# Kernel tuning notes

Measured on AMD Instinct MI355X. Metric: run time of the kernel, lower is better.

The kernel has to match this reference:

```python
import jax, jax.numpy as jnp
import numpy as np

B, T, H, L = 256, 1024, 64, 5  # batch, seq_len, hidden_size, num_layers


def setup_inputs() -> dict:
    key = jax.random.key(0)
    ks = jax.random.split(key, 10)
    s = 1.0 / np.sqrt(H)  # PyTorch LSTM/Linear uniform init bound

    def u(k, shape):
        return jax.random.uniform(k, shape, jnp.float32, -s, s)

    return {
        "x": jax.random.normal(ks[0], (B, T, 1), jnp.float32),
        "w_ih0": u(ks[1], (4 * H, 1)),          # layer 0 input weights (input_size=1)
        "w_ih_rest": u(ks[2], (L - 1, 4 * H, H)),  # layers 1..4 input weights
        "w_hh": u(ks[3], (L, 4 * H, H)),
        "b_ih": u(ks[4], (L, 4 * H)),
        "b_hh": u(ks[5], (L, 4 * H)),
        "W1": u(ks[6], (H, H)),
        "b1": u(ks[7], (H,)),
        "W2": u(ks[8], (1, H)),
        "b2": u(ks[9], (1,)),
        "future": 0,
    }


def _lstm_layer(x, w_ih, w_hh, b_ih, b_hh):
    # x: [B, T, in]; PyTorch gate order i, f, g, o
    gx = jnp.einsum('bti,gi->btg', x, w_ih) + b_ih  # precompute input projections [B,T,4H]
    h0 = jnp.zeros((x.shape[0], w_hh.shape[1]), x.dtype)

    def step(carry, gxt):
        h, c = carry
        gates = gxt + h @ w_hh.T + b_hh  # [B,4H]
        i, f, g, o = jnp.split(gates, 4, axis=-1)
        c = jax.nn.sigmoid(f) * c + jax.nn.sigmoid(i) * jnp.tanh(g)
        h = jax.nn.sigmoid(o) * jnp.tanh(c)
        return (h, c), h

    _, hs = jax.lax.scan(step, (h0, h0), jnp.swapaxes(gx, 0, 1))  # scan over time
    return jnp.swapaxes(hs, 0, 1)  # [B,T,H]


def _model(x, w_ih0, w_ih_rest, w_hh, b_ih, b_hh, W1, b1, W2, b2):
    # 5-layer LSTM (inter-layer dropout=0.1 is inactive in eval mode)
    h = _lstm_layer(x, w_ih0, w_hh[0], b_ih[0], b_hh[0])
    for l in range(1, w_hh.shape[0]):
        h = _lstm_layer(h, w_ih_rest[l - 1], w_hh[l], b_ih[l], b_hh[l])
    h = jax.nn.relu(h)
    h = jax.nn.relu(h @ W1.T + b1)
    return h @ W2.T + b2  # [B,T,1]


def reference(x, w_ih0, w_ih_rest, w_hh, b_ih, b_hh, W1, b1, W2, b2, future):
    out = None
    for _ in range(future + 1):
        out = _model(x, w_ih0, w_ih_rest, w_hh, b_ih, b_hh, W1, b1, W2, b2)
        x = jnp.concatenate([x, out[:, -1:, :]], axis=1)
    return out
```

## Files before the change

kernel.cpp:

```cpp
#include <hip/hip_runtime.h>

#define B_ 256
#define T_ 1024
#define H_ 64

typedef float f32x2 __attribute__((ext_vector_type(2)));
typedef float f32x4 __attribute__((ext_vector_type(4)));

__device__ __forceinline__ float fast_sigmoid(float x) {
    float e = __builtin_amdgcn_exp2f(-1.4426950408889634f * x);
    return __builtin_amdgcn_rcpf(1.0f + e);
}
__device__ __forceinline__ float fast_tanh(float x) {
    float e = __builtin_amdgcn_exp2f(2.8853900817779268f * x);
    return 1.0f - 2.0f * __builtin_amdgcn_rcpf(1.0f + e);
}

template<int CTRL>
__device__ __forceinline__ float dpp_addf(float v) {
    int vi = __builtin_bit_cast(int, v);
    int sh = __builtin_amdgcn_update_dpp(0, vi, CTRL, 0xF, 0xF, true);
    return v + __builtin_bit_cast(float, sh);
}

__device__ __forceinline__ void block_sync_lds() {
    asm volatile("s_waitcnt lgkmcnt(0)\n\ts_barrier" ::: "memory");
}

__device__ __forceinline__ float hsum4(f32x4 v) { return (v.x + v.y) + (v.z + v.w); }

__device__ __forceinline__ void load_w_heavy(const float* __restrict__ w_ih,
                                             const float* __restrict__ w_hh,
                                             int j, int kc, f32x4 wt[4][8]) {
    #pragma unroll
    for (int r = 0; r < 4; ++r) {
        const int row = r * H_ + j;
        const float* base = (kc < 2) ? (w_ih + row * H_ + kc * 32)
                                     : (w_hh + row * H_ + (kc - 2) * 32);
        #pragma unroll
        for (int q = 0; q < 8; ++q)
            wt[r][q] = *(const f32x4*)(base + 4 * q);
    }
    #pragma unroll
    for (int r = 0; r < 4; ++r)
        #pragma unroll
        for (int q = 0; q < 8; ++q)
            asm volatile("" : "+v"(wt[r][q]));
}

__device__ __forceinline__ void dot4x32(const float* chunk, const f32x4 wt[4][8],
                                        float acc[4]) {
    const f32x4* xv = (const f32x4*)chunk;
    f32x4 a0 = {0,0,0,0}, a1 = {0,0,0,0}, a2 = {0,0,0,0}, a3 = {0,0,0,0};
    #pragma unroll
    for (int q = 0; q < 8; ++q) {
        f32x4 hq = xv[q];
        a0 = __builtin_elementwise_fma(wt[0][q], hq, a0);
        a1 = __builtin_elementwise_fma(wt[1][q], hq, a1);
        a2 = __builtin_elementwise_fma(wt[2][q], hq, a2);
        a3 = __builtin_elementwise_fma(wt[3][q], hq, a3);
    }
    acc[0] = hsum4(a0); acc[1] = hsum4(a1);
    acc[2] = hsum4(a2); acc[3] = hsum4(a3);
}

__global__ __attribute__((amdgpu_flat_work_group_size(768, 768)))
void lstm_tri012(const float* __restrict__ x,
                 float* __restrict__ hout,
                 const float* __restrict__ w_ih0,
                 const float* __restrict__ whh0,
                 const float* __restrict__ bih0, const float* __restrict__ bhh0,
                 const float* __restrict__ wih1, const float* __restrict__ whh1,
                 const float* __restrict__ bih1, const float* __restrict__ bhh1,
                 const float* __restrict__ wih2, const float* __restrict__ whh2,
                 const float* __restrict__ bih2, const float* __restrict__ bhh2)
{
    const int b    = blockIdx.x;
    const int tid  = threadIdx.x;
    const int role = tid >> 8;
    const int loc  = tid & 255;
    const int kc   = loc & 3;
    const int j    = loc >> 2;

    __shared__ __align__(16) float bufL0[2][80];
    __shared__ __align__(16) float bufL1[2][144];
    __shared__ __align__(16) float bufL2[2][144];

    f32x4 wt[4][8];
    float bias0 = 0.f, bias1 = 0.f, bias2 = 0.f, bias3 = 0.f;
    float w00 = 0.f, w01 = 0.f, w02 = 0.f, w03 = 0.f;

    if (role == 0) {
        #pragma unroll
        for (int r = 0; r < 4; ++r) {
            const int row = r * H_ + j;
            const float* base = whh0 + row * H_ + kc * 16;
            #pragma unroll
            for (int q = 0; q < 4; ++q)
                wt[r][q] = *(const f32x4*)(base + 4 * q);
        }
        #pragma unroll
        for (int r = 0; r < 4; ++r)
            #pragma unroll
            for (int q = 0; q < 4; ++q)
                asm volatile("" : "+v"(wt[r][q]));
        if (kc == 0) {
            bias0 = bih0[0*H_+j] + bhh0[0*H_+j];
            bias1 = bih0[1*H_+j] + bhh0[1*H_+j];
            bias2 = bih0[2*H_+j] + bhh0[2*H_+j];
            bias3 = bih0[3*H_+j] + bhh0[3*H_+j];
            w00 = w_ih0[0*H_+j]; w01 = w_ih0[1*H_+j];
            w02 = w_ih0[2*H_+j]; w03 = w_ih0[3*H_+j];
        }
    } else {
        const float* wih = (role == 1) ? wih1 : wih2;
        const float* whh = (role == 1) ? whh1 : whh2;
        const float* bih = (role == 1) ? bih1 : bih2;
        const float* bhh = (role == 1) ? bhh1 : bhh2;
        load_w_heavy(wih, whh, j, kc, wt);
        if (kc == 0) {
            bias0 = bih[0*H_+j] + bhh[0*H_+j];
            bias1 = bih[1*H_+j] + bhh[1*H_+j];
            bias2 = bih[2*H_+j] + bhh[2*H_+j];
            bias3 = bih[3*H_+j] + bhh[3*H_+j];
        }
    }
    float c_st = 0.f;
    float xt = (role == 0) ? x[(long)b * T_] : 0.f;

    float (*myBuf)[144] = (role == 1) ? bufL1 : bufL2;

    if (loc < H_) {
        const int u = loc;
        if (role == 0)      bufL0[0][(u >> 4) * 20 + (u & 15)] = 0.f;
        else if (role == 1) bufL1[1][(2 + (u >> 5)) * 36 + (u & 31)] = 0.f;
        else                bufL2[0][(2 + (u >> 5)) * 36 + (u & 31)] = 0.f;
    }
    block_sync_lds();

    for (int s = 0; s <= T_ + 1; ++s) {
        const int rb = s & 1, wb = rb ^ 1;
        const bool active = (role == 0) ? (s < T_)
                          : (role == 1) ? (s >= 1 && s <= T_)
                                        : (s >= 2);
        if (active) {
            if (role == 0) {
                float xn = 0.f;
                if (s + 1 < T_) xn = x[(long)b * T_ + s + 1];
                const f32x4* xv = (const f32x4*)&bufL0[rb][kc * 20];
                f32x4 h0 = xv[0], h1 = xv[1], h2 = xv[2], h3 = xv[3];
                f32x4 a0 = {0,0,0,0}, a1 = {0,0,0,0}, a2 = {0,0,0,0}, a3 = {0,0,0,0};
                a0 = __builtin_elementwise_fma(wt[0][0], h0, a0);
                a1 = __builtin_elementwise_fma(wt[1][0], h0, a1);
                a2 = __builtin_elementwise_fma(wt[2][0], h0, a2);
                a3 = __builtin_elementwise_fma(wt[3][0], h0, a3);
                a0 = __builtin_elementwise_fma(wt[0][1], h1, a0);
                a1 = __builtin_elementwise_fma(wt[1][1], h1, a1);
                a2 = __builtin_elementwise_fma(wt[2][1], h1, a2);
                a3 = __builtin_elementwise_fma(wt[3][1], h1, a3);
                a0 = __builtin_elementwise_fma(wt[0][2], h2, a0);
                a1 = __builtin_elementwise_fma(wt[1][2], h2, a1);
                a2 = __builtin_elementwise_fma(wt[2][2], h2, a2);
                a3 = __builtin_elementwise_fma(wt[3][2], h2, a3);
                a0 = __builtin_elementwise_fma(wt[0][3], h3, a0);
                a1 = __builtin_elementwise_fma(wt[1][3], h3, a1);
                a2 = __builtin_elementwise_fma(wt[2][3], h3, a2);
                a3 = __builtin_elementwise_fma(wt[3][3], h3, a3);
                float acc0 = hsum4(a0), acc1 = hsum4(a1);
                float acc2 = hsum4(a2), acc3 = hsum4(a3);
                acc0 = dpp_addf<0xB1>(acc0); acc1 = dpp_addf<0xB1>(acc1);
                acc2 = dpp_addf<0xB1>(acc2); acc3 = dpp_addf<0xB1>(acc3);
                acc0 = dpp_addf<0x4E>(acc0); acc1 = dpp_addf<0x4E>(acc1);
                acc2 = dpp_addf<0x4E>(acc2); acc3 = dpp_addf<0x4E>(acc3);
                if (kc == 0) {
                    float i_ = fast_sigmoid(acc0 + bias0 + w00 * xt);
                    float f_ = fast_sigmoid(acc1 + bias1 + w01 * xt);
                    float g_ = fast_tanh   (acc2 + bias2 + w02 * xt);
                    float o_ = fast_sigmoid(acc3 + bias3 + w03 * xt);
                    c_st = f_ * c_st + i_ * g_;
                    float h = o_ * fast_tanh(c_st);
                    bufL0[wb][(j >> 4) * 20 + (j & 15)] = h;
                    bufL1[wb][(j >> 5) * 36 + (j & 31)] = h;
                }
                xt = xn;
            } else {
                float acc[4];
                dot4x32(&myBuf[rb][kc * 36], wt, acc);
                acc[0] = dpp_addf<0xB1>(acc[0]); acc[1] = dpp_addf<0xB1>(acc[1]);
                acc[2] = dpp_addf<0xB1>(acc[2]); acc[3] = dpp_addf<0xB1>(acc[3]);
                acc[0] = dpp_addf<0x4E>(acc[0]); acc[1] = dpp_addf<0x4E>(acc[1]);
                acc[2] = dpp_addf<0x4E>(acc[2]); acc[3] = dpp_addf<0x4E>(acc[3]);
                if (kc == 0) {
                    float i_ = fast_sigmoid(acc[0] + bias0);
                    float f_ = fast_sigmoid(acc[1] + bias1);
                    float g_ = fast_tanh   (acc[2] + bias2);
                    float o_ = fast_sigmoid(acc[3] + bias3);
                    c_st = f_ * c_st + i_ * g_;
                    float h = o_ * fast_tanh(c_st);
                    myBuf[wb][(2 + (j >> 5)) * 36 + (j & 31)] = h;
                    if (role == 1)
                        bufL2[wb][(j >> 5) * 36 + (j & 31)] = h;
                    else
                        hout[((long)b * T_ + (s - 2)) * H_ + j] = h;
                }
            }
        }
        block_sync_lds();
    }
}

__global__ __attribute__((amdgpu_flat_work_group_size(512, 512)))
void lstm_pair34(const float* __restrict__ xin,
                 float* __restrict__ hout,
                 const float* __restrict__ wih3, const float* __restrict__ whh3,
                 const float* __restrict__ bih3, const float* __restrict__ bhh3,
                 const float* __restrict__ wih4, const float* __restrict__ whh4,
                 const float* __restrict__ bih4, const float* __restrict__ bhh4)
{
    const int b    = blockIdx.x;
    const int tid  = threadIdx.x;
    const int role = tid >> 8;
    const int loc  = tid & 255;
    const int kc   = loc & 3;
    const int j    = loc >> 2;

    __shared__ __align__(16) float bufL3[2][144];
    __shared__ __align__(16) float bufL4[2][144];

    const float* wih = (role == 0) ? wih3 : wih4;
    const float* whh = (role == 0) ? whh3 : whh4;
    const float* bih = (role == 0) ? bih3 : bih4;
    const float* bhh = (role == 0) ? bhh3 : bhh4;
    float (*myBuf)[144] = (role == 0) ? bufL3 : bufL4;

    f32x4 wt[4][8];
    load_w_heavy(wih, whh, j, kc, wt);

    float bias0 = 0.f, bias1 = 0.f, bias2 = 0.f, bias3 = 0.f;
    if (kc == 0) {
        bias0 = bih[0*H_+j] + bhh[0*H_+j];
        bias1 = bih[1*H_+j] + bhh[1*H_+j];
        bias2 = bih[2*H_+j] + bhh[2*H_+j];
        bias3 = bih[3*H_+j] + bhh[3*H_+j];
    }
    float c_st = 0.f;

    if (tid < H_) {
        const int u = tid;
        bufL3[0][(u >> 5) * 36 + (u & 31)] = xin[(long)b * T_ * H_ + u];
        bufL3[0][(2 + (u >> 5)) * 36 + (u & 31)] = 0.f;
    } else if (tid < 128) {
        const int u = tid - 64;
        bufL4[1][(2 + (u >> 5)) * 36 + (u & 31)] = 0.f;
    }
    block_sync_lds();

    for (int s = 0; s <= T_; ++s) {
        const int rb = s & 1, wb = rb ^ 1;
        const bool active = (role == 0) ? (s < T_) : (s >= 1);
        if (active) {
            float xn = 0.f;
            if (role == 0 && kc == 1 && s + 1 < T_)
                xn = xin[((long)b * T_ + s + 1) * H_ + j];

            float acc[4];
            dot4x32(&myBuf[rb][kc * 36], wt, acc);
            acc[0] = dpp_addf<0xB1>(acc[0]); acc[1] = dpp_addf<0xB1>(acc[1]);
            acc[2] = dpp_addf<0xB1>(acc[2]); acc[3] = dpp_addf<0xB1>(acc[3]);
            acc[0] = dpp_addf<0x4E>(acc[0]); acc[1] = dpp_addf<0x4E>(acc[1]);
            acc[2] = dpp_addf<0x4E>(acc[2]); acc[3] = dpp_addf<0x4E>(acc[3]);

            if (kc == 0) {
                float i_ = fast_sigmoid(acc[0] + bias0);
                float f_ = fast_sigmoid(acc[1] + bias1);
                float g_ = fast_tanh   (acc[2] + bias2);
                float o_ = fast_sigmoid(acc[3] + bias3);
                c_st = f_ * c_st + i_ * g_;
                float h = o_ * fast_tanh(c_st);
                myBuf[wb][(2 + (j >> 5)) * 36 + (j & 31)] = h;
                if (role == 0)
                    bufL4[wb][(j >> 5) * 36 + (j & 31)] = h;
                else
                    hout[((long)b * T_ + (s - 1)) * H_ + j] = h;
            }
            if (role == 0 && kc == 1)
                bufL3[wb][(j >> 5) * 36 + (j & 31)] = xn;
        }
        block_sync_lds();
    }
}

__global__ __launch_bounds__(256)
void mlp_head_v2(const float* __restrict__ hbuf,
                 const float* __restrict__ W1,
                 const float* __restrict__ b1,
                 const float* __restrict__ W2,
                 const float* __restrict__ b2,
                 float* __restrict__ out)
{
    const long r = (long)blockIdx.x * 256 + threadIdx.x;

    float row[H_];
    const float4* src = (const float4*)(hbuf + r * H_);
    #pragma unroll
    for (int q = 0; q < 16; ++q) {
        float4 v = src[q];
        row[4*q+0] = fmaxf(v.x, 0.f); row[4*q+1] = fmaxf(v.y, 0.f);
        row[4*q+2] = fmaxf(v.z, 0.f); row[4*q+3] = fmaxf(v.w, 0.f);
    }
    #pragma unroll
    for (int q = 0; q < 16; ++q)
        asm volatile("" : "+v"(row[4*q]), "+v"(row[4*q+1]),
                         "+v"(row[4*q+2]), "+v"(row[4*q+3]));

    float acc = b2[0];
    for (int jj = 0; jj < H_; ++jj) {
        const float* wrow = W1 + jj * H_;
        float s0 = 0.f, s1 = 0.f, s2 = 0.f, s3 = 0.f;
        #pragma unroll
        for (int q = 0; q < 16; ++q) {
            s0 += row[4*q+0] * wrow[4*q+0];
            s1 += row[4*q+1] * wrow[4*q+1];
            s2 += row[4*q+2] * wrow[4*q+2];
            s3 += row[4*q+3] * wrow[4*q+3];
        }
        float y = fmaxf(b1[jj] + (s0 + s1) + (s2 + s3), 0.f);
        acc += y * W2[jj];
    }
    out[r] = acc;
}

extern "C" void kernel_launch(void* const* d_in, const int* in_sizes, int n_in,
                              void* d_out, int out_size, void* d_ws, size_t ws_size,
                              hipStream_t stream) {
    const float* x     = (const float*)d_in[0];
    const float* w_ih0 = (const float*)d_in[1];
    const float* w_ihr = (const float*)d_in[2];
    const float* w_hh  = (const float*)d_in[3];
    const float* b_ih  = (const float*)d_in[4];
    const float* b_hh  = (const float*)d_in[5];
    const float* W1    = (const float*)d_in[6];
    const float* b1    = (const float*)d_in[7];
    const float* W2    = (const float*)d_in[8];
    const float* b2    = (const float*)d_in[9];

    float* out = (float*)d_out;
    float* buf = (float*)d_ws;

    const long LW = 4L * H_ * H_;
    const long LB = 4L * H_;

    lstm_tri012<<<dim3(B_), dim3(768), 0, stream>>>(
        x, buf,
        w_ih0, w_hh + 0 * LW, b_ih + 0 * LB, b_hh + 0 * LB,
        w_ihr + 0 * LW, w_hh + 1 * LW, b_ih + 1 * LB, b_hh + 1 * LB,
        w_ihr + 1 * LW, w_hh + 2 * LW, b_ih + 2 * LB, b_hh + 2 * LB);

    lstm_pair34<<<dim3(B_), dim3(512), 0, stream>>>(
        buf, buf,
        w_ihr + 2 * LW, w_hh + 3 * LW, b_ih + 3 * LB, b_hh + 3 * LB,
        w_ihr + 3 * LW, w_hh + 4 * LW, b_ih + 4 * LB, b_hh + 4 * LB);

    mlp_head_v2<<<dim3((B_ * T_) / 256), dim3(256), 0, stream>>>(
        buf, W1, b1, W2, b2, out);
}
```

Measured before the change: 1.717 ms.

## Replace block-wide barriers with per-wave LDS counters and 4-deep ring buffers

```diff
diff --git a/kernel.cpp b/kernel.cpp
--- a/kernel.cpp
+++ b/kernel.cpp
@@ -23,11 +23,23 @@
     return v + __builtin_bit_cast(float, sh);
 }
 
-__device__ __forceinline__ void block_sync_lds() {
-    asm volatile("s_waitcnt lgkmcnt(0)\n\ts_barrier" ::: "memory");
-}
-
 __device__ __forceinline__ float hsum4(f32x4 v) { return (v.x + v.y) + (v.z + v.w); }
+
+__device__ __forceinline__ unsigned min4v(const volatile unsigned* c) {
+    unsigned a = c[0], b = c[1], d = c[2], e = c[3];
+    asm volatile("" ::: "memory");
+    unsigned m0 = a < b ? a : b;
+    unsigned m1 = d < e ? d : e;
+    return m0 < m1 ? m0 : m1;
+}
+__device__ __forceinline__ void wait_ge(const volatile unsigned* c, unsigned tgt) {
+    while (min4v(c) < tgt) {}
+}
+__device__ __forceinline__ void publish_cnt(volatile unsigned* slot, unsigned v,
+                                            bool lane0) {
+    asm volatile("s_waitcnt lgkmcnt(0)" ::: "memory");
+    if (lane0) *slot = v;
+}
 
 __device__ __forceinline__ void load_w_heavy(const float* __restrict__ w_ih,
                                              const float* __restrict__ w_hh,
@@ -81,10 +93,13 @@
     const int loc  = tid & 255;
     const int kc   = loc & 3;
     const int j    = loc >> 2;
-
-    __shared__ __align__(16) float bufL0[2][80];
-    __shared__ __align__(16) float bufL1[2][144];
-    __shared__ __align__(16) float bufL2[2][144];
+    const int wv   = (tid >> 6) & 3;
+    const bool lane0 = (tid & 63) == 0;
+
+    __shared__ __align__(16) float bufL0[4][80];
+    __shared__ __align__(16) float bufL1[4][144];
+    __shared__ __align__(16) float bufL2[4][144];
+    __shared__ __align__(16) unsigned cnts[3][4];
 
     f32x4 wt[4][8];
     float bias0 = 0.f, bias1 = 0.f, bias2 = 0.f, bias3 = 0.f;
@@ -125,87 +140,120 @@
             bias3 = bih[3*H_+j] + bhh[3*H_+j];
         }
     }
-    float c_st = 0.f;
-    float xt = (role == 0) ? x[(long)b * T_] : 0.f;
-
-    float (*myBuf)[144] = (role == 1) ? bufL1 : bufL2;
-
+
+    if (tid < 12) cnts[tid >> 2][tid & 3] = 0;
     if (loc < H_) {
         const int u = loc;
         if (role == 0)      bufL0[0][(u >> 4) * 20 + (u & 15)] = 0.f;
-        else if (role == 1) bufL1[1][(2 + (u >> 5)) * 36 + (u & 31)] = 0.f;
+        else if (role == 1) bufL1[0][(2 + (u >> 5)) * 36 + (u & 31)] = 0.f;
         else                bufL2[0][(2 + (u >> 5)) * 36 + (u & 31)] = 0.f;
     }
-    block_sync_lds();
-
-    for (int s = 0; s <= T_ + 1; ++s) {
-        const int rb = s & 1, wb = rb ^ 1;
-        const bool active = (role == 0) ? (s < T_)
-                          : (role == 1) ? (s >= 1 && s <= T_)
-                                        : (s >= 2);
-        if (active) {
-            if (role == 0) {
-                float xn = 0.f;
-                if (s + 1 < T_) xn = x[(long)b * T_ + s + 1];
-                const f32x4* xv = (const f32x4*)&bufL0[rb][kc * 20];
-                f32x4 h0 = xv[0], h1 = xv[1], h2 = xv[2], h3 = xv[3];
-                f32x4 a0 = {0,0,0,0}, a1 = {0,0,0,0}, a2 = {0,0,0,0}, a3 = {0,0,0,0};
-                a0 = __builtin_elementwise_fma(wt[0][0], h0, a0);
-                a1 = __builtin_elementwise_fma(wt[1][0], h0, a1);
-                a2 = __builtin_elementwise_fma(wt[2][0], h0, a2);
-                a3 = __builtin_elementwise_fma(wt[3][0], h0, a3);
-                a0 = __builtin_elementwise_fma(wt[0][1], h1, a0);
-                a1 = __builtin_elementwise_fma(wt[1][1], h1, a1);
-                a2 = __builtin_elementwise_fma(wt[2][1], h1, a2);
-                a3 = __builtin_elementwise_fma(wt[3][1], h1, a3);
-                a0 = __builtin_elementwise_fma(wt[0][2], h2, a0);
-                a1 = __builtin_elementwise_fma(wt[1][2], h2, a1);
-                a2 = __builtin_elementwise_fma(wt[2][2], h2, a2);
-                a3 = __builtin_elementwise_fma(wt[3][2], h2, a3);
-                a0 = __builtin_elementwise_fma(wt[0][3], h3, a0);
-                a1 = __builtin_elementwise_fma(wt[1][3], h3, a1);
-                a2 = __builtin_elementwise_fma(wt[2][3], h3, a2);
-                a3 = __builtin_elementwise_fma(wt[3][3], h3, a3);
-                float acc0 = hsum4(a0), acc1 = hsum4(a1);
-                float acc2 = hsum4(a2), acc3 = hsum4(a3);
-                acc0 = dpp_addf<0xB1>(acc0); acc1 = dpp_addf<0xB1>(acc1);
-                acc2 = dpp_addf<0xB1>(acc2); acc3 = dpp_addf<0xB1>(acc3);
-                acc0 = dpp_addf<0x4E>(acc0); acc1 = dpp_addf<0x4E>(acc1);
-                acc2 = dpp_addf<0x4E>(acc2); acc3 = dpp_addf<0x4E>(acc3);
-                if (kc == 0) {
-                    float i_ = fast_sigmoid(acc0 + bias0 + w00 * xt);
-                    float f_ = fast_sigmoid(acc1 + bias1 + w01 * xt);
-                    float g_ = fast_tanh   (acc2 + bias2 + w02 * xt);
-                    float o_ = fast_sigmoid(acc3 + bias3 + w03 * xt);
-                    c_st = f_ * c_st + i_ * g_;
-                    float h = o_ * fast_tanh(c_st);
-                    bufL0[wb][(j >> 4) * 20 + (j & 15)] = h;
-                    bufL1[wb][(j >> 5) * 36 + (j & 31)] = h;
-                }
-                xt = xn;
-            } else {
-                float acc[4];
-                dot4x32(&myBuf[rb][kc * 36], wt, acc);
-                acc[0] = dpp_addf<0xB1>(acc[0]); acc[1] = dpp_addf<0xB1>(acc[1]);
-                acc[2] = dpp_addf<0xB1>(acc[2]); acc[3] = dpp_addf<0xB1>(acc[3]);
-                acc[0] = dpp_addf<0x4E>(acc[0]); acc[1] = dpp_addf<0x4E>(acc[1]);
-                acc[2] = dpp_addf<0x4E>(acc[2]); acc[3] = dpp_addf<0x4E>(acc[3]);
-                if (kc == 0) {
-                    float i_ = fast_sigmoid(acc[0] + bias0);
-                    float f_ = fast_sigmoid(acc[1] + bias1);
-                    float g_ = fast_tanh   (acc[2] + bias2);
-                    float o_ = fast_sigmoid(acc[3] + bias3);
-                    c_st = f_ * c_st + i_ * g_;
-                    float h = o_ * fast_tanh(c_st);
-                    myBuf[wb][(2 + (j >> 5)) * 36 + (j & 31)] = h;
-                    if (role == 1)
-                        bufL2[wb][(j >> 5) * 36 + (j & 31)] = h;
-                    else
-                        hout[((long)b * T_ + (s - 2)) * H_ + j] = h;
-                }
-            }
-        }
-        block_sync_lds();
+    __syncthreads();
+
+    if (role == 0) {
+        float c_st = 0.f;
+        float xt = x[(long)b * T_];
+        unsigned bp = 0;
+        for (int t = 0; t < T_; ++t) {
+            float xn = 0.f;
+            if (t + 1 < T_) xn = x[(long)b * T_ + t + 1];
+            wait_ge(cnts[0], (unsigned)t);
+            if (t >= 4) {
+                const unsigned need = (unsigned)(t - 3);
+                while (bp < need) bp = min4v(cnts[1]);
+            }
+            const f32x4* xv = (const f32x4*)&bufL0[t & 3][kc * 20];
+            f32x4 h0 = xv[0], h1 = xv[1], h2 = xv[2], h3 = xv[3];
+            f32x4 a0 = {0,0,0,0}, a1 = {0,0,0,0}, a2 = {0,0,0,0}, a3 = {0,0,0,0};
+            a0 = __builtin_elementwise_fma(wt[0][0], h0, a0);
+            a1 = __builtin_elementwise_fma(wt[1][0], h0, a1);
+            a2 = __builtin_elementwise_fma(wt[2][0], h0, a2);
+            a3 = __builtin_elementwise_fma(wt[3][0], h0, a3);
+            a0 = __builtin_elementwise_fma(wt[0][1], h1, a0);
+            a1 = __builtin_elementwise_fma(wt[1][1], h1, a1);
+            a2 = __builtin_elementwise_fma(wt[2][1], h1, a2);
+            a3 = __builtin_elementwise_fma(wt[3][1], h1, a3);
+            a0 = __builtin_elementwise_fma(wt[0][2], h2, a0);
+            a1 = __builtin_elementwise_fma(wt[1][2], h2, a1);
+            a2 = __builtin_elementwise_fma(wt[2][2], h2, a2);
+            a3 = __builtin_elementwise_fma(wt[3][2], h2, a3);
+            a0 = __builtin_elementwise_fma(wt[0][3], h3, a0);
+            a1 = __builtin_elementwise_fma(wt[1][3], h3, a1);
+            a2 = __builtin_elementwise_fma(wt[2][3], h3, a2);
+            a3 = __builtin_elementwise_fma(wt[3][3], h3, a3);
+            float acc0 = hsum4(a0), acc1 = hsum4(a1);
+            float acc2 = hsum4(a2), acc3 = hsum4(a3);
+            acc0 = dpp_addf<0xB1>(acc0); acc1 = dpp_addf<0xB1>(acc1);
+            acc2 = dpp_addf<0xB1>(acc2); acc3 = dpp_addf<0xB1>(acc3);
+            acc0 = dpp_addf<0x4E>(acc0); acc1 = dpp_addf<0x4E>(acc1);
+            acc2 = dpp_addf<0x4E>(acc2); acc3 = dpp_addf<0x4E>(acc3);
+            if (kc == 0) {
+                float i_ = fast_sigmoid(acc0 + bias0 + w00 * xt);
+                float f_ = fast_sigmoid(acc1 + bias1 + w01 * xt);
+                float g_ = fast_tanh   (acc2 + bias2 + w02 * xt);
+                float o_ = fast_sigmoid(acc3 + bias3 + w03 * xt);
+                c_st = f_ * c_st + i_ * g_;
+                float h = o_ * fast_tanh(c_st);
+                bufL0[(t + 1) & 3][(j >> 4) * 20 + (j & 15)] = h;
+                bufL1[t & 3][(j >> 5) * 36 + (j & 31)] = h;
+            }
+            publish_cnt(&cnts[0][wv], (unsigned)(t + 1), lane0);
+            xt = xn;
+        }
+    } else if (role == 1) {
+        float c_st = 0.f;
+        unsigned pp = 0, bp = 0;
+        for (int t = 0; t < T_; ++t) {
+            wait_ge(cnts[1], (unsigned)t);
+            { const unsigned need = (unsigned)(t + 1);
+              while (pp < need) pp = min4v(cnts[0]); }
+            if (t >= 4) {
+                const unsigned need = (unsigned)(t - 3);
+                while (bp < need) bp = min4v(cnts[2]);
+            }
+            float acc[4];
+            dot4x32(&bufL1[t & 3][kc * 36], wt, acc);
+            acc[0] = dpp_addf<0xB1>(acc[0]); acc[1] = dpp_addf<0xB1>(acc[1]);
+            acc[2] = dpp_addf<0xB1>(acc[2]); acc[3] = dpp_addf<0xB1>(acc[3]);
+            acc[0] = dpp_addf<0x4E>(acc[0]); acc[1] = dpp_addf<0x4E>(acc[1]);
+            acc[2] = dpp_addf<0x4E>(acc[2]); acc[3] = dpp_addf<0x4E>(acc[3]);
+            if (kc == 0) {
+                float i_ = fast_sigmoid(acc[0] + bias0);
+                float f_ = fast_sigmoid(acc[1] + bias1);
+                float g_ = fast_tanh   (acc[2] + bias2);
+                float o_ = fast_sigmoid(acc[3] + bias3);
+                c_st = f_ * c_st + i_ * g_;
+                float h = o_ * fast_tanh(c_st);
+                bufL1[(t + 1) & 3][(2 + (j >> 5)) * 36 + (j & 31)] = h;
+                bufL2[t & 3][(j >> 5) * 36 + (j & 31)] = h;
+            }
+            publish_cnt(&cnts[1][wv], (unsigned)(t + 1), lane0);
+        }
+    } else {
+        float c_st = 0.f;
+        unsigned pp = 0;
+        for (int t = 0; t < T_; ++t) {
+            wait_ge(cnts[2], (unsigned)t);
+            { const unsigned need = (unsigned)(t + 1);
+              while (pp < need) pp = min4v(cnts[1]); }
+            float acc[4];
+            dot4x32(&bufL2[t & 3][kc * 36], wt, acc);
+            acc[0] = dpp_addf<0xB1>(acc[0]); acc[1] = dpp_addf<0xB1>(acc[1]);
+            acc[2] = dpp_addf<0xB1>(acc[2]); acc[3] = dpp_addf<0xB1>(acc[3]);
+            acc[0] = dpp_addf<0x4E>(acc[0]); acc[1] = dpp_addf<0x4E>(acc[1]);
+            acc[2] = dpp_addf<0x4E>(acc[2]); acc[3] = dpp_addf<0x4E>(acc[3]);
+            if (kc == 0) {
+                float i_ = fast_sigmoid(acc[0] + bias0);
+                float f_ = fast_sigmoid(acc[1] + bias1);
+                float g_ = fast_tanh   (acc[2] + bias2);
+                float o_ = fast_sigmoid(acc[3] + bias3);
+                c_st = f_ * c_st + i_ * g_;
+                float h = o_ * fast_tanh(c_st);
+                bufL2[(t + 1) & 3][(2 + (j >> 5)) * 36 + (j & 31)] = h;
+                hout[((long)b * T_ + t) * H_ + j] = h;
+            }
+            publish_cnt(&cnts[2][wv], (unsigned)(t + 1), lane0);
+        }
     }
 }
 
@@ -223,15 +271,17 @@
     const int loc  = tid & 255;
     const int kc   = loc & 3;
     const int j    = loc >> 2;
-
-    __shared__ __align__(16) float bufL3[2][144];
-    __shared__ __align__(16) float bufL4[2][144];
+    const int wv   = (tid >> 6) & 3;
+    const bool lane0 = (tid & 63) == 0;
+
+    __shared__ __align__(16) float bufL3[4][144];
+    __shared__ __align__(16) float bufL4[4][144];
+    __shared__ __align__(16) unsigned cnts[2][4];
 
     const float* wih = (role == 0) ? wih3 : wih4;
     const float* whh = (role == 0) ? whh3 : whh4;
     const float* bih = (role == 0) ? bih3 : bih4;
     const float* bhh = (role == 0) ? bhh3 : bhh4;
-    float (*myBuf)[144] = (role == 0) ? bufL3 : bufL4;
 
     f32x4 wt[4][8];
     load_w_heavy(wih, whh, j, kc, wt);
@@ -243,33 +293,36 @@
         bias2 = bih[2*H_+j] + bhh[2*H_+j];
         bias3 = bih[3*H_+j] + bhh[3*H_+j];
     }
-    float c_st = 0.f;
-
+
+    if (tid < 8) cnts[tid >> 2][tid & 3] = 0;
     if (tid < H_) {
         const int u = tid;
         bufL3[0][(u >> 5) * 36 + (u & 31)] = xin[(long)b * T_ * H_ + u];
         bufL3[0][(2 + (u >> 5)) * 36 + (u & 31)] = 0.f;
     } else if (tid < 128) {
         const int u = tid - 64;
-        bufL4[1][(2 + (u >> 5)) * 36 + (u & 31)] = 0.f;
-    }
-    block_sync_lds();
-
-    for (int s = 0; s <= T_; ++s) {
-        const int rb = s & 1, wb = rb ^ 1;
-        const bool active = (role == 0) ? (s < T_) : (s >= 1);
-        if (active) {
+        bufL4[0][(2 + (u >> 5)) * 36 + (u & 31)] = 0.f;
+    }
+    __syncthreads();
+
+    float c_st = 0.f;
+    if (role == 0) {
+        unsigned bp = 0;
+        for (int t = 0; t < T_; ++t) {
             float xn = 0.f;
-            if (role == 0 && kc == 1 && s + 1 < T_)
-                xn = xin[((long)b * T_ + s + 1) * H_ + j];
-
+            if (kc == 1 && t + 1 < T_)
+                xn = xin[((long)b * T_ + t + 1) * H_ + j];
+            wait_ge(cnts[0], (unsigned)t);
+            if (t >= 4) {
+                const unsigned need = (unsigned)(t - 3);
+                while (bp < need) bp = min4v(cnts[1]);
+            }
             float acc[4];
-            dot4x32(&myBuf[rb][kc * 36], wt, acc);
+            dot4x32(&bufL3[t & 3][kc * 36], wt, acc);
             acc[0] = dpp_addf<0xB1>(acc[0]); acc[1] = dpp_addf<0xB1>(acc[1]);
             acc[2] = dpp_addf<0xB1>(acc[2]); acc[3] = dpp_addf<0xB1>(acc[3]);
             acc[0] = dpp_addf<0x4E>(acc[0]); acc[1] = dpp_addf<0x4E>(acc[1]);
             acc[2] = dpp_addf<0x4E>(acc[2]); acc[3] = dpp_addf<0x4E>(acc[3]);
-
             if (kc == 0) {
                 float i_ = fast_sigmoid(acc[0] + bias0);
                 float f_ = fast_sigmoid(acc[1] + bias1);
@@ -277,16 +330,37 @@
                 float o_ = fast_sigmoid(acc[3] + bias3);
                 c_st = f_ * c_st + i_ * g_;
                 float h = o_ * fast_tanh(c_st);
-                myBuf[wb][(2 + (j >> 5)) * 36 + (j & 31)] = h;
-                if (role == 0)
-                    bufL4[wb][(j >> 5) * 36 + (j & 31)] = h;
-                else
-                    hout[((long)b * T_ + (s - 1)) * H_ + j] = h;
-            }
-            if (role == 0 && kc == 1)
-                bufL3[wb][(j >> 5) * 36 + (j & 31)] = xn;
-        }
-        block_sync_lds();
+                bufL3[(t + 1) & 3][(2 + (j >> 5)) * 36 + (j & 31)] = h;
+                bufL4[t & 3][(j >> 5) * 36 + (j & 31)] = h;
+            }
+            if (kc == 1)
+                bufL3[(t + 1) & 3][(j >> 5) * 36 + (j & 31)] = xn;
+            publish_cnt(&cnts[0][wv], (unsigned)(t + 1), lane0);
+        }
+    } else {
+        unsigned pp = 0;
+        for (int t = 0; t < T_; ++t) {
+            wait_ge(cnts[1], (unsigned)t);
+            { const unsigned need = (unsigned)(t + 1);
+              while (pp < need) pp = min4v(cnts[0]); }
+            float acc[4];
+            dot4x32(&bufL4[t & 3][kc * 36], wt, acc);
+            acc[0] = dpp_addf<0xB1>(acc[0]); acc[1] = dpp_addf<0xB1>(acc[1]);
+            acc[2] = dpp_addf<0xB1>(acc[2]); acc[3] = dpp_addf<0xB1>(acc[3]);
+            acc[0] = dpp_addf<0x4E>(acc[0]); acc[1] = dpp_addf<0x4E>(acc[1]);
+            acc[2] = dpp_addf<0x4E>(acc[2]); acc[3] = dpp_addf<0x4E>(acc[3]);
+            if (kc == 0) {
+                float i_ = fast_sigmoid(acc[0] + bias0);
+                float f_ = fast_sigmoid(acc[1] + bias1);
+                float g_ = fast_tanh   (acc[2] + bias2);
+                float o_ = fast_sigmoid(acc[3] + bias3);
+                c_st = f_ * c_st + i_ * g_;
+                float h = o_ * fast_tanh(c_st);
+                bufL4[(t + 1) & 3][(2 + (j >> 5)) * 36 + (j & 31)] = h;
+                hout[((long)b * T_ + t) * H_ + j] = h;
+            }
+            publish_cnt(&cnts[1][wv], (unsigned)(t + 1), lane0);
+        }
     }
 }
 
```

Result: slower. 3.178 ms (+85.0%).
